# Kernel tuning notes

Measured on AMD Instinct MI355X. Metric: run time of the kernel, lower is better.

Reference implementation:

```python
import jax, jax.numpy as jnp
import numpy as np

B, S, D, H = 8, 4096, 1024, 16
DH = D // H  # head size = 64


def setup_inputs() -> dict:
    key = jax.random.key(0)
    ks = jax.random.split(key, 9)
    scale = 1.0 / np.sqrt(D)
    x = jax.random.normal(ks[0], (B, S, D), dtype=jnp.float32)
    wq = jax.random.normal(ks[1], (D, D), dtype=jnp.float32) * scale
    bq = jnp.zeros((D,), dtype=jnp.float32)
    wk = jax.random.normal(ks[2], (D, D), dtype=jnp.float32) * scale
    bk = jnp.zeros((D,), dtype=jnp.float32)
    wv = jax.random.normal(ks[3], (D, D), dtype=jnp.float32) * scale
    bv = jnp.zeros((D,), dtype=jnp.float32)
    wo = jax.random.normal(ks[4], (D, D), dtype=jnp.float32) * scale
    bo = jnp.zeros((D,), dtype=jnp.float32)
    return {"x": x, "wq": wq, "bq": bq, "wk": wk, "bk": bk,
            "wv": wv, "bv": bv, "wo": wo, "bo": bo}


def reference(x, wq, bq, wk, bk, wv, bv, wo, bo):
    b, s, d = x.shape
    # torch Linear: y = x @ W^T + b
    q = (x @ wq.T + bq).reshape(b, s, H, DH)
    k = (x @ wk.T + bk).reshape(b, s, H, DH)
    v = (x @ wv.T + bv).reshape(b, s, H, DH)
    # NOTE: original transpose_for_scores only reshapes (no permute), so
    # matmul(q, k.transpose(-1,-2)) contracts over head_size and the softmax
    # runs over the HEAD axis per token: scores shape [B, S, H, H].
    scores = jnp.einsum('bshd,bsgd->bshg', q, k) / jnp.sqrt(jnp.float32(DH))
    probs = jax.nn.softmax(scores, axis=-1)
    ctx = jnp.einsum('bshg,bsgd->bshd', probs, v).reshape(b, s, d)
    return ctx @ wo.T + bo
```

## Files before the change

kernel.cpp:

```cpp
#include <hip/hip_runtime.h>
#include <hip/hip_bf16.h>


#define DEV static __device__ __forceinline__

typedef __attribute__((ext_vector_type(8))) _Float16 fp16x8;
typedef __attribute__((ext_vector_type(4))) float f32x4;

DEV unsigned short f2h(float f) {
    union { _Float16 h; unsigned short u; } c;
    c.h = (_Float16)f;
    return c.u;
}

DEV void gl_lds16(const void* g, void* l) {
    __builtin_amdgcn_global_load_lds(
        (const __attribute__((address_space(1))) unsigned int*)g,
        (__attribute__((address_space(3))) unsigned int*)l, 16, 0, 0);
}

__global__ __launch_bounds__(256) void k_convert(
    const float* __restrict__ x,
    const float* __restrict__ wq, const float* __restrict__ wk,
    const float* __restrict__ wv, const float* __restrict__ wo,
    const float* __restrict__ bq, const float* __restrict__ bk,
    const float* __restrict__ bv,
    unsigned short* __restrict__ Xb, unsigned short* __restrict__ Wb,
    unsigned short* __restrict__ Wob, float* __restrict__ biasc)
{
    const int NX = 33554432 / 4;
    const int NW = 3145728 / 4;
    const int NO = 1048576 / 4;
    const int NB = 3072 / 4;
    const int total = NX + NW + NO + NB;
    for (int c = blockIdx.x * blockDim.x + threadIdx.x; c < total;
         c += gridDim.x * blockDim.x) {
        if (c < NX) {
            float4 v = ((const float4*)x)[c];
            uint2 u;
            u.x = f2h(v.x) | ((unsigned int)f2h(v.y) << 16);
            u.y = f2h(v.z) | ((unsigned int)f2h(v.w) << 16);
            ((uint2*)Xb)[c] = u;
        } else if (c < NX + NW) {
            int e = c - NX;
            const float* w = (e < 262144) ? wq : (e < 524288) ? wk : wv;
            int off = e & 262143;
            float4 v = ((const float4*)w)[off];
            uint2 u;
            u.x = f2h(v.x) | ((unsigned int)f2h(v.y) << 16);
            u.y = f2h(v.z) | ((unsigned int)f2h(v.w) << 16);
            ((uint2*)Wb)[e] = u;
        } else if (c < NX + NW + NO) {
            int e = c - NX - NW;
            float4 v = ((const float4*)wo)[e];
            uint2 u;
            u.x = f2h(v.x) | ((unsigned int)f2h(v.y) << 16);
            u.y = f2h(v.z) | ((unsigned int)f2h(v.w) << 16);
            ((uint2*)Wob)[e] = u;
        } else {
            int e = c - NX - NW - NO;
            const float* b = (e < 256) ? bq : (e < 512) ? bk : bv;
            int off = e & 255;
            ((float4*)biasc)[e] = ((const float4*)b)[off];
        }
    }
}

template <int MODE>
DEV void g256_tile(const unsigned short* __restrict__ Ac,
                   const unsigned short* __restrict__ Bc,
                   unsigned short* As_stg, unsigned short* Bs_stg,
                   const unsigned short* gA, const unsigned short* gB,
                   int tid, int rA, int rB, int c0, int c1,
                   f32x4 (&acc)[8][4])
{
    fp16x8 a0[8], b0[4];
#pragma unroll
    for (int i = 0; i < 8; ++i)
        a0[i] = *(const fp16x8*)(const void*)&Ac[rA + i * 1024 + c0];
#pragma unroll
    for (int j = 0; j < 4; ++j)
        b0[j] = *(const fp16x8*)(const void*)&Bc[rB + j * 1024 + c0];
#pragma unroll
    for (int i = 0; i < 8; ++i)
#pragma unroll
        for (int j = 0; j < 4; ++j)
            acc[i][j] = __builtin_amdgcn_mfma_f32_16x16x32_f16(a0[i], b0[j], acc[i][j], 0, 0, 0);

    fp16x8 a1[8], b1[4];
#pragma unroll
    for (int i = 0; i < 8; ++i)
        a1[i] = *(const fp16x8*)(const void*)&Ac[rA + i * 1024 + c1];
#pragma unroll
    for (int j = 0; j < 4; ++j)
        b1[j] = *(const fp16x8*)(const void*)&Bc[rB + j * 1024 + c1];

    asm volatile("s_waitcnt lgkmcnt(0)" ::: "memory");
    __builtin_amdgcn_sched_barrier(0);
    __builtin_amdgcn_s_barrier();
    asm volatile("" ::: "memory");

    if (MODE == 0) {
#pragma unroll
        for (int s = 0; s < 4; ++s) {
            gl_lds16(gA + (size_t)s * 65536, (char*)As_stg + (tid + s * 512) * 16);
            gl_lds16(gB + (size_t)s * 65536, (char*)Bs_stg + (tid + s * 512) * 16);
        }
        __builtin_amdgcn_sched_barrier(0);
    }

    __builtin_amdgcn_s_setprio(1);
#pragma unroll
    for (int i = 0; i < 8; ++i)
#pragma unroll
        for (int j = 0; j < 4; ++j)
            acc[i][j] = __builtin_amdgcn_mfma_f32_16x16x32_f16(a1[i], b1[j], acc[i][j], 0, 0, 0);
    __builtin_amdgcn_s_setprio(0);

    if (MODE == 0) asm volatile("s_waitcnt vmcnt(8)" ::: "memory");
    if (MODE == 1) asm volatile("s_waitcnt vmcnt(0)" ::: "memory");
    if (MODE != 2) {
        __builtin_amdgcn_s_barrier();
        asm volatile("" ::: "memory");
    }
}

template <bool OUT_F16>
__global__ __launch_bounds__(512, 2) void k_gemm256(
    const unsigned short* __restrict__ A,
    const unsigned short* __restrict__ B,
    const float* __restrict__ bias,
    unsigned short* __restrict__ Ch,
    float* __restrict__ Cf,
    int ldc, int nbx)
{
    __shared__ __align__(16) unsigned short As[2][256 * 64];
    __shared__ __align__(16) unsigned short Bs[2][256 * 64];

    const int tid  = threadIdx.x;
    const int lane = tid & 63;
    const int w    = tid >> 6;
    const int wr   = w >> 2, wc = w & 3;
    const int quad = lane >> 4;
    const int lr   = lane & 15;

    const int cpx = gridDim.x >> 3;
    const int id  = (blockIdx.x & 7) * cpx + (blockIdx.x >> 3);
    const int by  = id / nbx, bx = id - by * nbx;
    const int m0  = by * 256, n0 = bx * 256;

    const int srow = tid >> 3;
    const int kk   = (((tid & 7) ^ (srow & 7)) << 3);
    const unsigned short* gAp = A + (size_t)(m0 + srow) * 1024 + kk;
    const unsigned short* gBp = B + (size_t)(n0 + srow) * 1024 + kk;

    const int swz = (lr & 7) << 3;
    const int c0  = (quad * 8) ^ swz;
    const int c1  = c0 ^ 32;
    const int rA  = (wr * 128 + lr) * 64;
    const int rB  = (wc * 64 + lr) * 64;

    f32x4 acc[8][4];
#pragma unroll
    for (int i = 0; i < 8; ++i)
#pragma unroll
        for (int j = 0; j < 4; ++j) {
            f32x4 z = {0.f, 0.f, 0.f, 0.f};
            acc[i][j] = z;
        }

#pragma unroll
    for (int s = 0; s < 4; ++s) {
        gl_lds16(gAp + (size_t)s * 65536, (char*)As[0] + (tid + s * 512) * 16);
        gl_lds16(gBp + (size_t)s * 65536, (char*)Bs[0] + (tid + s * 512) * 16);
    }
#pragma unroll
    for (int s = 0; s < 4; ++s) {
        gl_lds16(gAp + (size_t)s * 65536 + 64, (char*)As[1] + (tid + s * 512) * 16);
        gl_lds16(gBp + (size_t)s * 65536 + 64, (char*)Bs[1] + (tid + s * 512) * 16);
    }
    asm volatile("s_waitcnt vmcnt(8)" ::: "memory");
    __builtin_amdgcn_s_barrier();
    asm volatile("" ::: "memory");

    const unsigned short* gAt = gAp + 128;
    const unsigned short* gBt = gBp + 128;
    for (int t = 0; t < 14; t += 2) {
        g256_tile<0>(As[0], Bs[0], As[0], Bs[0], gAt, gBt, tid, rA, rB, c0, c1, acc);
        gAt += 64; gBt += 64;
        g256_tile<0>(As[1], Bs[1], As[1], Bs[1], gAt, gBt, tid, rA, rB, c0, c1, acc);
        gAt += 64; gBt += 64;
    }
    g256_tile<1>(As[0], Bs[0], As[0], Bs[0], gAt, gBt, tid, rA, rB, c0, c1, acc);
    g256_tile<2>(As[1], Bs[1], As[1], Bs[1], gAt, gBt, tid, rA, rB, c0, c1, acc);

    float bj[4];
#pragma unroll
    for (int j = 0; j < 4; ++j) bj[j] = bias[n0 + wc * 64 + j * 16 + lr];
#pragma unroll
    for (int i = 0; i < 8; ++i) {
        const int mrow = m0 + wr * 128 + i * 16 + quad * 4;
#pragma unroll
        for (int j = 0; j < 4; ++j) {
            const int ncol = n0 + wc * 64 + j * 16 + lr;
#pragma unroll
            for (int r = 0; r < 4; ++r) {
                float v = acc[i][j][r] + bj[j];
                if (OUT_F16)
                    Ch[(size_t)(mrow + r) * ldc + ncol] = f2h(v);
                else
                    Cf[(size_t)(mrow + r) * ldc + ncol] = v;
            }
        }
    }
}

__global__ __launch_bounds__(256) void k_attn(
    const unsigned short* __restrict__ qkv,
    unsigned short* __restrict__ Ctx)
{
    __shared__ __align__(16) unsigned short sqk[4][32 * 72];
    __shared__ __align__(16) unsigned short svt[4][64 * 24];
    __shared__ __align__(16) unsigned short spp[4][16 * 24];

    const int tid  = threadIdx.x;
    const int wv   = tid >> 6;
    const int l    = tid & 63;
    const int t    = blockIdx.x * 4 + wv;
    const unsigned short* tok = qkv + (size_t)t * 3072;

    unsigned short* qk = sqk[wv];
    unsigned short* vt = svt[wv];
    unsigned short* pp = spp[wv];

    const int quad = l >> 4;
    const int lr   = l & 15;
    const int row8 = l >> 3;
    const int col8 = (l & 7) * 8;

#pragma unroll
    for (int i = 0; i < 4; ++i) {
        const int row = i * 8 + row8;
        uint4 u = *(const uint4*)(tok + i * 512 + l * 8);
        *(uint4*)&qk[row * 72 + col8] = u;
    }
#pragma unroll
    for (int i = 0; i < 2; ++i) {
        const int g = i * 8 + row8;
        uint4 u = *(const uint4*)(tok + 2048 + i * 512 + l * 8);
        const unsigned short* hu = (const unsigned short*)&u;
#pragma unroll
        for (int c = 0; c < 8; ++c)
            vt[(col8 + c) * 24 + g] = hu[c];
    }
    asm volatile("s_waitcnt lgkmcnt(0)" ::: "memory");

    f32x4 s = {0.f, 0.f, 0.f, 0.f};
#pragma unroll
    for (int ks = 0; ks < 2; ++ks) {
        fp16x8 aq = *(const fp16x8*)(const void*)&qk[lr * 72 + ks * 32 + quad * 8];
        fp16x8 bk = *(const fp16x8*)(const void*)&qk[(16 + lr) * 72 + ks * 32 + quad * 8];
        s = __builtin_amdgcn_mfma_f32_16x16x32_f16(aq, bk, s, 0, 0, 0);
    }

#pragma unroll
    for (int r = 0; r < 4; ++r) {
        float sv = s[r] * 0.125f;
        float m = sv;
        m = fmaxf(m, __shfl_xor(m, 1, 64));
        m = fmaxf(m, __shfl_xor(m, 2, 64));
        m = fmaxf(m, __shfl_xor(m, 4, 64));
        m = fmaxf(m, __shfl_xor(m, 8, 64));
        float e = __expf(sv - m);
        float su = e;
        su += __shfl_xor(su, 1, 64);
        su += __shfl_xor(su, 2, 64);
        su += __shfl_xor(su, 4, 64);
        su += __shfl_xor(su, 8, 64);
        float p = e * __builtin_amdgcn_rcpf(su);
        pp[(quad * 4 + r) * 24 + lr] = f2h(p);
    }
    asm volatile("s_waitcnt lgkmcnt(0)" ::: "memory");

    fp16x8 pa;
    if (quad < 2) {
        pa = *(const fp16x8*)(const void*)&pp[lr * 24 + quad * 8];
    } else {
#pragma unroll
        for (int j = 0; j < 8; ++j) pa[j] = (_Float16)0.f;
    }

    f32x4 c[4];
#pragma unroll
    for (int nb = 0; nb < 4; ++nb) {
        fp16x8 bv;
        if (quad < 2) {
            bv = *(const fp16x8*)(const void*)&vt[(nb * 16 + lr) * 24 + quad * 8];
        } else {
#pragma unroll
            for (int j = 0; j < 8; ++j) bv[j] = (_Float16)0.f;
        }
        f32x4 z = {0.f, 0.f, 0.f, 0.f};
        c[nb] = __builtin_amdgcn_mfma_f32_16x16x32_f16(pa, bv, z, 0, 0, 0);
    }
    asm volatile("s_waitcnt lgkmcnt(0)" ::: "memory");

#pragma unroll
    for (int nb = 0; nb < 4; ++nb)
#pragma unroll
        for (int r = 0; r < 4; ++r)
            qk[(quad * 4 + r) * 72 + nb * 16 + lr] = f2h(c[nb][r]);
    asm volatile("s_waitcnt lgkmcnt(0)" ::: "memory");

    unsigned short* dst = Ctx + (size_t)t * 1024;
#pragma unroll
    for (int i = 0; i < 2; ++i) {
        const int row = i * 8 + row8;
        uint4 u = *(const uint4*)&qk[row * 72 + col8];
        *(uint4*)(dst + row * 64 + col8) = u;
    }
}

extern "C" void kernel_launch(void* const* d_in, const int* in_sizes, int n_in,
                              void* d_out, int out_size, void* d_ws, size_t ws_size,
                              hipStream_t stream)
{
    (void)in_sizes; (void)n_in; (void)out_size;

    const float* x  = (const float*)d_in[0];
    const float* wq = (const float*)d_in[1];
    const float* bq = (const float*)d_in[2];
    const float* wk = (const float*)d_in[3];
    const float* bk = (const float*)d_in[4];
    const float* wv = (const float*)d_in[5];
    const float* bv = (const float*)d_in[6];
    const float* wo = (const float*)d_in[7];
    const float* bo = (const float*)d_in[8];

    if (ws_size < 276836352ull) return;

    char* ws = (char*)d_ws;
    unsigned short* QKV  = (unsigned short*)(ws);
    unsigned short* Xb   = (unsigned short*)(ws + 201326592);
    unsigned short* Wb   = (unsigned short*)(ws + 268435456);
    unsigned short* Wob  = (unsigned short*)(ws + 274726912);
    float*          bqkv = (float*)(ws + 276824064);
    unsigned short* Ctx  = Xb;

    k_convert<<<2048, 256, 0, stream>>>(x, wq, wk, wv, wo, bq, bk, bv,
                                        Xb, Wb, Wob, bqkv);
    k_gemm256<true><<<1536, 512, 0, stream>>>(
        Xb, Wb, bqkv, QKV, nullptr, 3072, 12);
    k_attn<<<8192, 256, 0, stream>>>(QKV, Ctx);
    k_gemm256<false><<<512, 512, 0, stream>>>(
        Ctx, Wob, bo, nullptr, (float*)d_out, 1024, 4);
}
```

Measured before the change: 592.4 us.

## Restructure GEMM mainloop into 4-stage K=32 ring with register double-buffered fragments

Replaces the 2-buffer K=64 LDS pipeline with a 4-stage ring of K=32 slices. The A and next-tile B fragments are double-buffered in registers, and global-to-LDS loads and LDS reads are interleaved between two half-MFMA phases within each k-tile. The goal is to hide LDS read latency and global load latency behind MFMA issue and to shorten the exposed waits at barriers. In exchange it drops the XOR swizzle layout, which may add LDS bank conflicts, and it adds two barriers per smaller k-step.

```diff
diff --git a/kernel.cpp b/kernel.cpp
--- a/kernel.cpp
+++ b/kernel.cpp
@@ -6,6 +6,8 @@
 
 typedef __attribute__((ext_vector_type(8))) _Float16 fp16x8;
 typedef __attribute__((ext_vector_type(4))) float f32x4;
+
+#define MFMA16(a, b, c) __builtin_amdgcn_mfma_f32_16x16x32_f16(a, b, c, 0, 0, 0)
 
 DEV unsigned short f2h(float f) {
     union { _Float16 h; unsigned short u; } c;
@@ -67,59 +69,51 @@
 }
 
 template <int MODE>
-DEV void g256_tile(const unsigned short* __restrict__ Ac,
-                   const unsigned short* __restrict__ Bc,
-                   unsigned short* As_stg, unsigned short* Bs_stg,
-                   const unsigned short* gA, const unsigned short* gB,
-                   int tid, int rA, int rB, int c0, int c1,
-                   f32x4 (&acc)[8][4])
-{
-    fp16x8 a0[8], b0[4];
-#pragma unroll
-    for (int i = 0; i < 8; ++i)
-        a0[i] = *(const fp16x8*)(const void*)&Ac[rA + i * 1024 + c0];
-#pragma unroll
-    for (int j = 0; j < 4; ++j)
-        b0[j] = *(const fp16x8*)(const void*)&Bc[rB + j * 1024 + c0];
-#pragma unroll
-    for (int i = 0; i < 8; ++i)
-#pragma unroll
-        for (int j = 0; j < 4; ++j)
-            acc[i][j] = __builtin_amdgcn_mfma_f32_16x16x32_f16(a0[i], b0[j], acc[i][j], 0, 0, 0);
-
-    fp16x8 a1[8], b1[4];
-#pragma unroll
-    for (int i = 0; i < 8; ++i)
-        a1[i] = *(const fp16x8*)(const void*)&Ac[rA + i * 1024 + c1];
-#pragma unroll
-    for (int j = 0; j < 4; ++j)
-        b1[j] = *(const fp16x8*)(const void*)&Bc[rB + j * 1024 + c1];
-
-    asm volatile("s_waitcnt lgkmcnt(0)" ::: "memory");
+DEV void g_ktile(
+    const unsigned short* rdA_d, const unsigned short* rdB_d,
+    const unsigned short* rdA_n, const unsigned short* rdB_n,
+    char* stA0, char* stA1, char* stB0, char* stB1,
+    const unsigned short* gA0, const unsigned short* gA1,
+    const unsigned short* gB0, const unsigned short* gB1,
+    fp16x8 (&Ac)[8], fp16x8 (&An)[8],
+    fp16x8 (&B01c)[2], fp16x8 (&B01n)[2],
+    f32x4 (&acc)[8][4])
+{
+    fp16x8 B23_0, B23_1;
+    if (MODE == 0) { gl_lds16(gA0, stA0); gl_lds16(gA1, stA1); }
+    B23_0 = *(const fp16x8*)(const void*)(rdB_d + 1024);
+    B23_1 = *(const fp16x8*)(const void*)(rdB_d + 1536);
     __builtin_amdgcn_sched_barrier(0);
-    __builtin_amdgcn_s_barrier();
-    asm volatile("" ::: "memory");
-
-    if (MODE == 0) {
-#pragma unroll
-        for (int s = 0; s < 4; ++s) {
-            gl_lds16(gA + (size_t)s * 65536, (char*)As_stg + (tid + s * 512) * 16);
-            gl_lds16(gB + (size_t)s * 65536, (char*)Bs_stg + (tid + s * 512) * 16);
-        }
-        __builtin_amdgcn_sched_barrier(0);
-    }
-
     __builtin_amdgcn_s_setprio(1);
 #pragma unroll
-    for (int i = 0; i < 8; ++i)
-#pragma unroll
-        for (int j = 0; j < 4; ++j)
-            acc[i][j] = __builtin_amdgcn_mfma_f32_16x16x32_f16(a1[i], b1[j], acc[i][j], 0, 0, 0);
+    for (int i = 0; i < 8; ++i) {
+        acc[i][0] = MFMA16(Ac[i], B01c[0], acc[i][0]);
+        acc[i][1] = MFMA16(Ac[i], B01c[1], acc[i][1]);
+    }
     __builtin_amdgcn_s_setprio(0);
-
+    __builtin_amdgcn_sched_barrier(0);
+    if (MODE == 0) { gl_lds16(gB0, stB0); gl_lds16(gB1, stB1); }
     if (MODE == 0) asm volatile("s_waitcnt vmcnt(8)" ::: "memory");
-    if (MODE == 1) asm volatile("s_waitcnt vmcnt(0)" ::: "memory");
-    if (MODE != 2) {
+    if (MODE == 1) asm volatile("s_waitcnt vmcnt(4)" ::: "memory");
+    if (MODE == 2) asm volatile("s_waitcnt vmcnt(0)" ::: "memory");
+    if (MODE != 3) {
+        __builtin_amdgcn_s_barrier();
+        asm volatile("" ::: "memory");
+#pragma unroll
+        for (int i = 0; i < 8; ++i)
+            An[i] = *(const fp16x8*)(const void*)(rdA_n + i * 512);
+        B01n[0] = *(const fp16x8*)(const void*)(rdB_n + 0);
+        B01n[1] = *(const fp16x8*)(const void*)(rdB_n + 512);
+    }
+    __builtin_amdgcn_sched_barrier(0);
+    __builtin_amdgcn_s_setprio(1);
+#pragma unroll
+    for (int i = 0; i < 8; ++i) {
+        acc[i][2] = MFMA16(Ac[i], B23_0, acc[i][2]);
+        acc[i][3] = MFMA16(Ac[i], B23_1, acc[i][3]);
+    }
+    __builtin_amdgcn_s_setprio(0);
+    if (MODE != 3) {
         __builtin_amdgcn_s_barrier();
         asm volatile("" ::: "memory");
     }
@@ -134,8 +128,8 @@
     float* __restrict__ Cf,
     int ldc, int nbx)
 {
-    __shared__ __align__(16) unsigned short As[2][256 * 64];
-    __shared__ __align__(16) unsigned short Bs[2][256 * 64];
+    __shared__ __align__(16) unsigned short Asx[4][2][4096];
+    __shared__ __align__(16) unsigned short Bsx[4][2][4096];
 
     const int tid  = threadIdx.x;
     const int lane = tid & 63;
@@ -149,16 +143,19 @@
     const int by  = id / nbx, bx = id - by * nbx;
     const int m0  = by * 256, n0 = bx * 256;
 
-    const int srow = tid >> 3;
-    const int kk   = (((tid & 7) ^ (srow & 7)) << 3);
-    const unsigned short* gAp = A + (size_t)(m0 + srow) * 1024 + kk;
-    const unsigned short* gBp = B + (size_t)(n0 + srow) * 1024 + kk;
-
-    const int swz = (lr & 7) << 3;
-    const int c0  = (quad * 8) ^ swz;
-    const int c1  = c0 ^ 32;
-    const int rA  = (wr * 128 + lr) * 64;
-    const int rB  = (wc * 64 + lr) * 64;
+    const unsigned short* rdA0 = &Asx[0][wr][0] + lr * 32 + quad * 8;
+    const unsigned short* rdB0 = &Bsx[0][wc >> 1][0] + (wc & 1) * 2048 + lr * 32 + quad * 8;
+    char* stA_base = (char*)&Asx[0][0][0] + tid * 16;
+    char* stB_base = (char*)&Bsx[0][0][0] + tid * 16;
+    const unsigned short* gA0 = A + (size_t)(m0 + (tid >> 2)) * 1024 + (tid & 3) * 8;
+    const unsigned short* gA1 = gA0 + (size_t)128 * 1024;
+    const unsigned short* gB0 = B + (size_t)(n0 + (tid >> 2)) * 1024 + (tid & 3) * 8;
+    const unsigned short* gB1 = gB0 + (size_t)128 * 1024;
+
+#define RD_A(d) (rdA0 + (d) * 8192)
+#define RD_B(d) (rdB0 + (d) * 8192)
+#define ST_A(d, h) (stA_base + ((d) * 2 + (h)) * 8192)
+#define ST_B(d, h) (stB_base + ((d) * 2 + (h)) * 8192)
 
     f32x4 acc[8][4];
 #pragma unroll
@@ -170,29 +167,57 @@
         }
 
 #pragma unroll
-    for (int s = 0; s < 4; ++s) {
-        gl_lds16(gAp + (size_t)s * 65536, (char*)As[0] + (tid + s * 512) * 16);
-        gl_lds16(gBp + (size_t)s * 65536, (char*)Bs[0] + (tid + s * 512) * 16);
-    }
-#pragma unroll
-    for (int s = 0; s < 4; ++s) {
-        gl_lds16(gAp + (size_t)s * 65536 + 64, (char*)As[1] + (tid + s * 512) * 16);
-        gl_lds16(gBp + (size_t)s * 65536 + 64, (char*)Bs[1] + (tid + s * 512) * 16);
+    for (int u = 0; u < 3; ++u) {
+        gl_lds16(gA0 + u * 32, ST_A(u, 0));
+        gl_lds16(gA1 + u * 32, ST_A(u, 1));
+        gl_lds16(gB0 + u * 32, ST_B(u, 0));
+        gl_lds16(gB1 + u * 32, ST_B(u, 1));
     }
     asm volatile("s_waitcnt vmcnt(8)" ::: "memory");
     __builtin_amdgcn_s_barrier();
     asm volatile("" ::: "memory");
 
-    const unsigned short* gAt = gAp + 128;
-    const unsigned short* gBt = gBp + 128;
-    for (int t = 0; t < 14; t += 2) {
-        g256_tile<0>(As[0], Bs[0], As[0], Bs[0], gAt, gBt, tid, rA, rB, c0, c1, acc);
-        gAt += 64; gBt += 64;
-        g256_tile<0>(As[1], Bs[1], As[1], Bs[1], gAt, gBt, tid, rA, rB, c0, c1, acc);
-        gAt += 64; gBt += 64;
-    }
-    g256_tile<1>(As[0], Bs[0], As[0], Bs[0], gAt, gBt, tid, rA, rB, c0, c1, acc);
-    g256_tile<2>(As[1], Bs[1], As[1], Bs[1], gAt, gBt, tid, rA, rB, c0, c1, acc);
+    fp16x8 Ar0[8], Ar1[8], B01a[2], B01b[2];
+#pragma unroll
+    for (int i = 0; i < 8; ++i)
+        Ar0[i] = *(const fp16x8*)(const void*)(RD_A(0) + i * 512);
+    B01a[0] = *(const fp16x8*)(const void*)(RD_B(0) + 0);
+    B01a[1] = *(const fp16x8*)(const void*)(RD_B(0) + 512);
+
+    const unsigned short *pA0 = gA0 + 96, *pA1 = gA1 + 96,
+                         *pB0 = gB0 + 96, *pB1 = gB1 + 96;
+    for (int it = 0; it < 7; ++it) {
+        g_ktile<0>(RD_A(0), RD_B(0), RD_A(1), RD_B(1),
+                   ST_A(3, 0), ST_A(3, 1), ST_B(3, 0), ST_B(3, 1),
+                   pA0, pA1, pB0, pB1, Ar0, Ar1, B01a, B01b, acc);
+        g_ktile<0>(RD_A(1), RD_B(1), RD_A(2), RD_B(2),
+                   ST_A(0, 0), ST_A(0, 1), ST_B(0, 0), ST_B(0, 1),
+                   pA0 + 32, pA1 + 32, pB0 + 32, pB1 + 32, Ar1, Ar0, B01b, B01a, acc);
+        g_ktile<0>(RD_A(2), RD_B(2), RD_A(3), RD_B(3),
+                   ST_A(1, 0), ST_A(1, 1), ST_B(1, 0), ST_B(1, 1),
+                   pA0 + 64, pA1 + 64, pB0 + 64, pB1 + 64, Ar0, Ar1, B01a, B01b, acc);
+        g_ktile<0>(RD_A(3), RD_B(3), RD_A(0), RD_B(0),
+                   ST_A(2, 0), ST_A(2, 1), ST_B(2, 0), ST_B(2, 1),
+                   pA0 + 96, pA1 + 96, pB0 + 96, pB1 + 96, Ar1, Ar0, B01b, B01a, acc);
+        pA0 += 128; pA1 += 128; pB0 += 128; pB1 += 128;
+    }
+    g_ktile<0>(RD_A(0), RD_B(0), RD_A(1), RD_B(1),
+               ST_A(3, 0), ST_A(3, 1), ST_B(3, 0), ST_B(3, 1),
+               pA0, pA1, pB0, pB1, Ar0, Ar1, B01a, B01b, acc);
+    g_ktile<1>(RD_A(1), RD_B(1), RD_A(2), RD_B(2),
+               ST_A(3, 0), ST_A(3, 1), ST_B(3, 0), ST_B(3, 1),
+               pA0, pA1, pB0, pB1, Ar1, Ar0, B01b, B01a, acc);
+    g_ktile<2>(RD_A(2), RD_B(2), RD_A(3), RD_B(3),
+               ST_A(3, 0), ST_A(3, 1), ST_B(3, 0), ST_B(3, 1),
+               pA0, pA1, pB0, pB1, Ar0, Ar1, B01a, B01b, acc);
+    g_ktile<3>(RD_A(3), RD_B(3), RD_A(0), RD_B(0),
+               ST_A(3, 0), ST_A(3, 1), ST_B(3, 0), ST_B(3, 1),
+               pA0, pA1, pB0, pB1, Ar1, Ar0, B01b, B01a, acc);
+
+#undef RD_A
+#undef RD_B
+#undef ST_A
+#undef ST_B
 
     float bj[4];
 #pragma unroll
@@ -260,7 +285,7 @@
     for (int ks = 0; ks < 2; ++ks) {
         fp16x8 aq = *(const fp16x8*)(const void*)&qk[lr * 72 + ks * 32 + quad * 8];
         fp16x8 bk = *(const fp16x8*)(const void*)&qk[(16 + lr) * 72 + ks * 32 + quad * 8];
-        s = __builtin_amdgcn_mfma_f32_16x16x32_f16(aq, bk, s, 0, 0, 0);
+        s = MFMA16(aq, bk, s);
     }
 
 #pragma unroll
@@ -301,7 +326,7 @@
             for (int j = 0; j < 8; ++j) bv[j] = (_Float16)0.f;
         }
         f32x4 z = {0.f, 0.f, 0.f, 0.f};
-        c[nb] = __builtin_amdgcn_mfma_f32_16x16x32_f16(pa, bv, z, 0, 0, 0);
+        c[nb] = MFMA16(pa, bv, z);
     }
     asm volatile("s_waitcnt lgkmcnt(0)" ::: "memory");
 
```

New measurement: 592.5 us. Within noise of the previous version (+0.0%).
